# Optimization experiments

Hardware: AMD Instinct MI355X
Metric: run time of the kernel (lower is better)

## Reference

```python
import jax, jax.numpy as jnp
import numpy as np

N, F, H, D = 50000, 128, 8, 16   # nodes, node features, heads, per-head dim (F == H*D -> Identity residual)
E, G = 800000, 512               # edges, graphs
HD = H * D


def _xavier(key, shape):
    fan = sum(shape[-2:]) if len(shape) >= 2 else shape[0] + 1
    lim = (6.0 / (shape[-2] + shape[-1])) ** 0.5 if len(shape) >= 2 else (6.0 / fan) ** 0.5
    return jax.random.uniform(key, shape, jnp.float32, -lim, lim)


def setup_inputs() -> dict:
    key = jax.random.key(0)
    ks = jax.random.split(key, 10)
    x = jax.random.normal(ks[0], (N, F), jnp.float32)
    edge_index = jax.random.randint(ks[1], (2, E), 0, N, dtype=jnp.int64)
    batch = jnp.sort(jax.random.randint(ks[2], (N,), 0, G, dtype=jnp.int64))
    W_src = _xavier(ks[3], (HD, F))
    W_dst = _xavier(ks[4], (HD, F))
    double_attn = _xavier(ks[5], (1, H, D))  # xavier over last two dims
    bias = jnp.zeros((HD,), jnp.float32)
    prelu_alpha = jnp.float32(0.25)          # nn.PReLU() default single weight
    w_weighting = _xavier(ks[6], (1, HD))
    b_weighting = jnp.zeros((1,), jnp.float32)
    w_score = _xavier(ks[7], (HD, HD))
    b_score = jnp.zeros((HD,), jnp.float32)
    return {
        "x": x, "edge_index": edge_index, "batch": batch,
        "W_src": W_src, "W_dst": W_dst, "double_attn": double_attn,
        "bias": bias, "prelu_alpha": prelu_alpha,
        "w_weighting": w_weighting, "b_weighting": b_weighting,
        "w_score": w_score, "b_score": b_score,
    }


def reference(x, edge_index, batch, W_src, W_dst, double_attn, bias, prelu_alpha,
              w_weighting, b_weighting, w_score, b_score):
    src, dst = edge_index[0], edge_index[1]
    # dropout is identity in eval mode
    src_p = (x @ W_src.T).reshape(N, H, D)    # [N,H,D]
    dst_p = (x @ W_dst.T).reshape(N, H, D)
    # edge-wise attention logits: gather + LeakyReLU(0.2) + dot with attention vector
    e = src_p[src] + dst_p[dst]               # [E,H,D]
    e = jnp.where(e > 0, e, 0.2 * e)
    logits = jnp.einsum('ehd,ohd->eh', e, double_attn)  # [E,H] (double_attn has leading 1)
    # segment softmax over destination nodes (global max shift, as in original)
    exp = jnp.exp(logits - logits.max())
    denom = jax.ops.segment_sum(exp, dst, num_segments=N)  # [N,H]
    alpha = exp / (denom[dst] + 1e-16)        # [E,H]
    # weighted aggregation of source projections
    msg = src_p[src] * alpha[:, :, None]      # [E,H,D]
    out = jax.ops.segment_sum(msg, dst, num_segments=N)    # [N,H,D]
    out = out + x.reshape(N, H, D)            # residual (Identity since F == H*D)
    out = out.reshape(N, HD) + bias           # concat heads + bias
    out = jnp.where(out > 0, out, prelu_alpha * out)       # PReLU activation
    # ReadoutPhase: gated sum pooling + max pooling per graph, concatenated
    weighted = jax.nn.sigmoid(out @ w_weighting.T + b_weighting)  # [N,1]
    score = out @ w_score.T + b_score                              # [N,HD]
    g_sum = jax.ops.segment_sum(weighted * score, batch, num_segments=G)  # [G,HD]
    g_max = jax.ops.segment_max(out, batch, num_segments=G)              # [G,HD]
    readout = jnp.concatenate([g_sum, g_max], axis=1)                     # [G,2*HD]
    return out, readout
```

## Files before the change

kernel.cpp:

```cpp
#include <hip/hip_runtime.h>

#define NODES 50000
#define FEAT 128
#define EDGES 800000
#define GRAPHS 512
#define NB 196
#define CHUNK 4096
#define ABLK 196
#define BCAP 8192
#define PROJ_BLOCKS 782

typedef unsigned int u32;
typedef unsigned short u16;
typedef __attribute__((ext_vector_type(8))) short short8;
typedef __attribute__((ext_vector_type(4))) float v4f;
typedef __attribute__((ext_vector_type(4))) u32 u32x4;
typedef __attribute__((ext_vector_type(2))) float f2;

static __device__ __forceinline__ float bflo(u32 u){ return __uint_as_float(u << 16); }
static __device__ __forceinline__ float bfhi(u32 u){ return __uint_as_float(u & 0xffff0000u); }
static __device__ __forceinline__ u16 f2bf(float f){
  u32 u = __float_as_uint(f);
  u32 r = u + 0x7fffu + ((u >> 16) & 1u);
  return (u16)(r >> 16);
}
static __device__ __forceinline__ u32 packbf(float a, float b){
  return (u32)f2bf(a) | ((u32)f2bf(b) << 16);
}
static __device__ __forceinline__ f2 unpk(u32 u){ f2 r; r.x = bflo(u); r.y = bfhi(u); return r; }
static __device__ __forceinline__ f2 vmax2(f2 a, f2 b){ f2 r; r.x = fmaxf(a.x,b.x); r.y = fmaxf(a.y,b.y); return r; }

#define LROW 68
__global__ __launch_bounds__(256) void proj_hist_kernel(
    const float* __restrict__ x, const float* __restrict__ Wsrc,
    const float* __restrict__ Wdst, u16* __restrict__ srcp, u16* __restrict__ dstp,
    const int* __restrict__ ei, int* __restrict__ bcount)
{
  __shared__ u32 x_lds[64 * LROW];
  __shared__ int cnt[NB];
  const int t = threadIdx.x;

  if (blockIdx.x >= PROJ_BLOCKS){
    const int b = blockIdx.x - PROJ_BLOCKS;
    for (int k = t; k < NB; k += 256) cnt[k] = 0;
    __syncthreads();
    const int e0 = b * CHUNK;
    const int e1 = (e0 + CHUNK < EDGES) ? e0 + CHUNK : EDGES;
    for (int e = e0 + t; e < e1; e += 256)
      atomicAdd(&cnt[ei[EDGES + e] >> 8], 1);
    __syncthreads();
    for (int k = t; k < NB; k += 256) bcount[b * NB + k] = cnt[k];
    return;
  }

  const int node0 = blockIdx.x * 64;
  const int rows_valid = NODES - node0 < 64 ? NODES - node0 : 64;
  const float4* xp = (const float4*)(x + (size_t)node0 * 128);
  for (int idx = t; idx < rows_valid * 32; idx += 256){
    const float4 v = xp[idx];
    const int row = idx >> 5, cq = idx & 31;
    x_lds[row * LROW + cq * 2]     = packbf(v.x, v.y);
    x_lds[row * LROW + cq * 2 + 1] = packbf(v.z, v.w);
  }

  const int wave = t >> 6, lane = t & 63;
  const int r16 = lane & 15;
  const int quad = lane >> 4;
  const int ko = quad * 4;
  const int n0 = wave * 32;

  short8 bs[2][4], bd[2][4];
  #pragma unroll
  for (int nt = 0; nt < 2; ++nt){
    const int col = n0 + nt * 16 + r16;
    #pragma unroll
    for (int k = 0; k < 4; ++k){
      const float4* wp = (const float4*)(Wsrc + col * 128 + quad * 8 + k * 32);
      float4 w0 = wp[0], w1 = wp[1];
      u32x4 pk; pk.x = packbf(w0.x,w0.y); pk.y = packbf(w0.z,w0.w);
      pk.z = packbf(w1.x,w1.y); pk.w = packbf(w1.z,w1.w);
      bs[nt][k] = __builtin_bit_cast(short8, pk);
      const float4* vp = (const float4*)(Wdst + col * 128 + quad * 8 + k * 32);
      float4 v0 = vp[0], v1 = vp[1];
      u32x4 qk; qk.x = packbf(v0.x,v0.y); qk.y = packbf(v0.z,v0.w);
      qk.z = packbf(v1.x,v1.y); qk.w = packbf(v1.z,v1.w);
      bd[nt][k] = __builtin_bit_cast(short8, qk);
    }
  }
  __syncthreads();

  #pragma unroll
  for (int mt = 0; mt < 4; ++mt){
    const int node_base = node0 + mt * 16;
    if (node_base >= NODES) break;
    short8 afr[4];
    #pragma unroll
    for (int k = 0; k < 4; ++k)
      afr[k] = *(const short8*)&x_lds[(mt * 16 + r16) * LROW + ko + k * 16];
    v4f s0 = {0.f,0.f,0.f,0.f}, s1 = s0, d0 = s0, d1 = s0;
    #pragma unroll
    for (int k = 0; k < 4; ++k){
      s0 = __builtin_amdgcn_mfma_f32_16x16x32_bf16(afr[k], bs[0][k], s0, 0, 0, 0);
      s1 = __builtin_amdgcn_mfma_f32_16x16x32_bf16(afr[k], bs[1][k], s1, 0, 0, 0);
      d0 = __builtin_amdgcn_mfma_f32_16x16x32_bf16(afr[k], bd[0][k], d0, 0, 0, 0);
      d1 = __builtin_amdgcn_mfma_f32_16x16x32_bf16(afr[k], bd[1][k], d1, 0, 0, 0);
    }
    u16* so = srcp + (size_t)(node_base + quad * 4) * 128 + n0 + r16;
    u16* do_ = dstp + (size_t)(node_base + quad * 4) * 128 + n0 + r16;
    #pragma unroll
    for (int r = 0; r < 4; ++r){
      so[r * 128]      = f2bf(s0[r]);
      so[r * 128 + 16] = f2bf(s1[r]);
      do_[r * 128]      = f2bf(d0[r]);
      do_[r * 128 + 16] = f2bf(d1[r]);
    }
  }
}

__global__ __launch_bounds__(256) void bucket_scatter_kernel(
    const int* __restrict__ ei, const int* __restrict__ bcount,
    int* __restrict__ bstart_g, u32* __restrict__ ebuf)
{
  __shared__ int tot[256];
  __shared__ int bstart_s[NB + 1];
  __shared__ int obase_s[NB];
  __shared__ int cur[NB];
  const int b = blockIdx.x, t = threadIdx.x;
  int total = 0, obase = 0;
  if (t < NB){
    int run = 0;
    for (int q = 0; q < ABLK; ++q){
      if (q == b) obase = run;
      run += bcount[q * NB + t];
    }
    total = run;
  }
  tot[t] = total;
  __syncthreads();
  const int v = total;
  for (int off = 1; off < 256; off <<= 1){
    const int add = (t >= off) ? tot[t - off] : 0;
    __syncthreads();
    tot[t] += add;
    __syncthreads();
  }
  if (t < NB){
    bstart_s[t] = tot[t] - v;
    obase_s[t] = obase;
    cur[t] = 0;
  }
  if (t == NB - 1) bstart_s[NB] = tot[t];
  __syncthreads();
  if (b == 0 && t <= NB) bstart_g[t] = bstart_s[t];

  const int e0 = b * CHUNK;
  const int e1 = (e0 + CHUNK < EDGES) ? e0 + CHUNK : EDGES;
  for (int e = e0 + t; e < e1; e += 256){
    const int d = ei[EDGES + e];
    const int s = ei[e];
    const int k = d >> 8;
    const int r = atomicAdd(&cur[k], 1);
    ebuf[bstart_s[k] + obase_s[k] + r] = (u32)s | ((u32)(d & 255) << 16);
  }
}

__global__ __launch_bounds__(256) void bucket_csr_kernel(
    const u32* __restrict__ ebuf, const int* __restrict__ bstart,
    int* __restrict__ row_start, int* __restrict__ srclist)
{
  __shared__ int cnt[256], excl[256], cur[256];
  __shared__ u32 loc[BCAP];
  const int k = blockIdx.x, t = threadIdx.x;
  const int base = bstart[k];
  int ne = bstart[k + 1] - base;
  if (ne > BCAP) ne = BCAP;
  cnt[t] = 0;
  __syncthreads();
  for (int j = t; j < ne; j += 256)
    atomicAdd(&cnt[(ebuf[base + j] >> 16) & 255], 1);
  __syncthreads();
  const int v = cnt[t];
  for (int off = 1; off < 256; off <<= 1){
    const int add = (t >= off) ? cnt[t - off] : 0;
    __syncthreads();
    cnt[t] += add;
    __syncthreads();
  }
  excl[t] = cnt[t] - v;
  cur[t] = cnt[t] - v;
  __syncthreads();
  const int node = k * 256 + t;
  if (node <= NODES) row_start[node] = base + excl[t];
  for (int j = t; j < ne; j += 256){
    const u32 e = ebuf[base + j];
    const int p = atomicAdd(&cur[(e >> 16) & 255], 1);
    loc[p] = e & 0xFFFFu;
  }
  __syncthreads();
  for (int j = t; j < ne; j += 256)
    srclist[base + j] = (int)loc[j];
}

__global__ __launch_bounds__(256, 4) void aggregate_kernel(
    const u16* __restrict__ srcp, const u16* __restrict__ dstp,
    const int* __restrict__ row_start, const int* __restrict__ srclist,
    const float* __restrict__ x, const float* __restrict__ attn,
    const float* __restrict__ bias, const float* __restrict__ palpha,
    const float* __restrict__ ww, const float* __restrict__ bw,
    float* __restrict__ outp, float* __restrict__ weighted)
{
  const int wv = threadIdx.x >> 6;
  const int lane = threadIdx.x & 63;
  const int half = lane >> 5;
  const int l32 = lane & 31;
  const int h = lane & 7;
  const int es = (lane >> 3) & 3;
  const int i = (blockIdx.x * 4 + wv) * 2 + half;
  const uint4* sp = (const uint4*)srcp;

  f2 d2[8], a2[8];
  {
    const uint4 dA = ((const uint4*)dstp)[(size_t)i * 16 + h * 2];
    const uint4 dB = ((const uint4*)dstp)[(size_t)i * 16 + h * 2 + 1];
    d2[0]=unpk(dA.x); d2[1]=unpk(dA.y); d2[2]=unpk(dA.z); d2[3]=unpk(dA.w);
    d2[4]=unpk(dB.x); d2[5]=unpk(dB.y); d2[6]=unpk(dB.z); d2[7]=unpk(dB.w);
    const float4* ap = (const float4*)attn + h * 4;
    #pragma unroll
    for (int q = 0; q < 4; ++q){
      const float4 vv = ap[q];
      a2[2*q].x = vv.x; a2[2*q].y = vv.y; a2[2*q+1].x = vv.z; a2[2*q+1].y = vv.w;
    }
  }
  const int lo = row_start[i], hi = row_start[i + 1];
  const int deg = hi - lo;
  int myidx = 0;
  if (l32 < deg) myidx = srclist[lo + l32];
  const int nb = (deg + 3) >> 2;
  int nbw = nb;
  { const int ot = __shfl_xor(nb, 32); nbw = nbw > ot ? nbw : ot; }

  f2 acc2[8];
  #pragma unroll
  for (int q = 0; q < 8; ++q){ acc2[q].x = 0.f; acc2[q].y = 0.f; }
  float denom = 0.f;

  auto LOADK = [&](int s, uint4& A, uint4& B){
    const uint4* rp = sp + (size_t)s * 16 + h * 2;
    A = rp[0]; B = rp[1];
  };
  auto COMPV = [&](bool valid, const uint4& A, const uint4& B){
    f2 sv[8];
    sv[0]=unpk(A.x); sv[1]=unpk(A.y); sv[2]=unpk(A.z); sv[3]=unpk(A.w);
    sv[4]=unpk(B.x); sv[5]=unpk(B.y); sv[6]=unpk(B.z); sv[7]=unpk(B.w);
    f2 p; p.x = 0.f; p.y = 0.f;
    #pragma unroll
    for (int q = 0; q < 8; ++q){
      f2 e = sv[q] + d2[q];
      e = vmax2(e, e * 0.2f);
      p += e * a2[q];
    }
    const float w = valid ? __expf(p.x + p.y) : 0.f;
    denom += w;
    f2 w2; w2.x = w; w2.y = w;
    #pragma unroll
    for (int q = 0; q < 8; ++q) acc2[q] += sv[q] * w2;
  };

  int s0,s1,s2,s3,s4,s5,s6,s7;
  {
    int t0;
    t0 = __shfl(myidx, half*32 +  0 + es); s0 = ( 0 + es < deg) ? t0 : 0;
    t0 = __shfl(myidx, half*32 +  4 + es); s1 = ( 4 + es < deg) ? t0 : 0;
    t0 = __shfl(myidx, half*32 +  8 + es); s2 = ( 8 + es < deg) ? t0 : 0;
    t0 = __shfl(myidx, half*32 + 12 + es); s3 = (12 + es < deg) ? t0 : 0;
    t0 = __shfl(myidx, half*32 + 16 + es); s4 = (16 + es < deg) ? t0 : 0;
    t0 = __shfl(myidx, half*32 + 20 + es); s5 = (20 + es < deg) ? t0 : 0;
    t0 = __shfl(myidx, half*32 + 24 + es); s6 = (24 + es < deg) ? t0 : 0;
    t0 = __shfl(myidx, half*32 + 28 + es); s7 = (28 + es < deg) ? t0 : 0;
  }

  uint4 A0,B0,A1,B1,A2,B2,A3,B3;
  if (nbw > 0) LOADK(s0, A0, B0);
  if (nbw > 1) LOADK(s1, A1, B1);
  if (nbw > 2) LOADK(s2, A2, B2);
  if (nbw > 3) LOADK(s3, A3, B3);
  if (nbw > 0){ COMPV( 0 + es < deg, A0, B0); if (nbw > 4) LOADK(s4, A0, B0); }
  if (nbw > 1){ COMPV( 4 + es < deg, A1, B1); if (nbw > 5) LOADK(s5, A1, B1); }
  if (nbw > 2){ COMPV( 8 + es < deg, A2, B2); if (nbw > 6) LOADK(s6, A2, B2); }
  if (nbw > 3){ COMPV(12 + es < deg, A3, B3); if (nbw > 7) LOADK(s7, A3, B3); }
  if (nbw > 4) COMPV(16 + es < deg, A0, B0);
  if (nbw > 5) COMPV(20 + es < deg, A1, B1);
  if (nbw > 6) COMPV(24 + es < deg, A2, B2);
  if (nbw > 7) COMPV(28 + es < deg, A3, B3);
  if (nbw > 8){
    for (int kk = 8; kk < nbw; ++kk){
      const int il = kk * 4 + es;
      const int s = (il < deg) ? srclist[lo + il] : 0;
      uint4 TA, TB;
      LOADK(s, TA, TB);
      COMPV(il < deg, TA, TB);
    }
  }

  #pragma unroll
  for (int m = 8; m <= 16; m <<= 1){
    #pragma unroll
    for (int q = 0; q < 8; ++q){
      acc2[q].x += __shfl_xor(acc2[q].x, m);
      acc2[q].y += __shfl_xor(acc2[q].y, m);
    }
    denom += __shfl_xor(denom, m);
  }
  const float inv = 1.f / (denom + 1e-16f);

  const float al = palpha[0];
  float o[16];
  {
    const float4* xp = (const float4*)x + (size_t)i * 32 + h * 4;
    const float4* bp = (const float4*)bias + h * 4;
    #pragma unroll
    for (int q = 0; q < 4; ++q){
      const float4 xv = xp[q];
      const float4 bv = bp[q];
      float t0 = fmaf(acc2[2*q].x,   inv, xv.x) + bv.x;
      float t1 = fmaf(acc2[2*q].y,   inv, xv.y) + bv.y;
      float t2 = fmaf(acc2[2*q+1].x, inv, xv.z) + bv.z;
      float t3 = fmaf(acc2[2*q+1].y, inv, xv.w) + bv.w;
      o[4*q]   = (t0 > 0.f) ? t0 : al * t0;
      o[4*q+1] = (t1 > 0.f) ? t1 : al * t1;
      o[4*q+2] = (t2 > 0.f) ? t2 : al * t2;
      o[4*q+3] = (t3 > 0.f) ? t3 : al * t3;
    }
  }
  if (es == 0){
    float4* op = (float4*)outp + (size_t)i * 32 + h * 4;
    #pragma unroll
    for (int q = 0; q < 4; ++q){
      float4 vv; vv.x = o[4*q]; vv.y = o[4*q+1]; vv.z = o[4*q+2]; vv.w = o[4*q+3];
      op[q] = vv;
    }
  }
  float z = 0.f;
  {
    const float4* gp = (const float4*)ww + h * 4;
    #pragma unroll
    for (int q = 0; q < 4; ++q){
      const float4 gv = gp[q];
      z = fmaf(o[4*q], gv.x, z); z = fmaf(o[4*q+1], gv.y, z);
      z = fmaf(o[4*q+2], gv.z, z); z = fmaf(o[4*q+3], gv.w, z);
    }
  }
  z += __shfl_xor(z, 1);
  z += __shfl_xor(z, 2);
  z += __shfl_xor(z, 4);
  if (l32 == 0){
    z += bw[0];
    weighted[i] = 1.f / (1.f + __expf(-z));
  }
}

__global__ __launch_bounds__(256) void readout_kernel(
    const float* __restrict__ outp, const float* __restrict__ weighted,
    const int* __restrict__ batchv, const float* __restrict__ wscore,
    const float* __restrict__ bscore, float* __restrict__ ro)
{
  __shared__ int range_s[2];
  __shared__ float wsum_s[128];
  __shared__ float max_s[128];
  __shared__ float wtot_s[2];
  __shared__ float part_s[256];
  const int g = blockIdx.x, t = threadIdx.x;
  const int col = t & 127, grp = t >> 7;
  if (t < 2){
    const int target = g + t;
    int lo = 0, hi = NODES;
    while (lo < hi){ const int m = (lo + hi) >> 1; if (batchv[m] < target) lo = m + 1; else hi = m; }
    range_s[t] = lo;
  }
  __syncthreads();
  const int lo = range_s[0], hi = range_s[1];
  float acc = 0.f, vmax = -INFINITY, wacc = 0.f;
  for (int n = lo + grp; n < hi; n += 2){
    const float w = weighted[n];
    const float v = outp[n * 128 + col];
    acc = fmaf(w, v, acc);
    vmax = fmaxf(vmax, v);
    if (col == 0) wacc += w;
  }
  part_s[t] = acc;
  if (col == 0) wtot_s[grp] = wacc;
  __syncthreads();
  if (grp == 0) wsum_s[col] = acc + part_s[col + 128];
  __syncthreads();
  part_s[t] = vmax;
  __syncthreads();
  if (grp == 0) max_s[col] = fmaxf(vmax, part_s[col + 128]);
  const float wtot = wtot_s[0] + wtot_s[1];
  __syncthreads();
  float dot = 0.f;
  const float* wr = wscore + col * 128 + grp * 64;
  const float* xs = wsum_s + grp * 64;
  #pragma unroll
  for (int k = 0; k < 64; ++k) dot = fmaf(wr[k], xs[k], dot);
  part_s[t] = dot;
  __syncthreads();
  if (grp == 0){
    const float s = dot + part_s[col + 128] + wtot * bscore[col];
    ro[g * 256 + col] = s;
    ro[g * 256 + 128 + col] = max_s[col];
  }
}

extern "C" void kernel_launch(void* const* d_in, const int* in_sizes, int n_in,
                              void* d_out, int out_size, void* d_ws, size_t ws_size,
                              hipStream_t stream)
{
  const float* x      = (const float*)d_in[0];
  const int*   ei     = (const int*)d_in[1];
  const int*   batchv = (const int*)d_in[2];
  const float* Wsrc   = (const float*)d_in[3];
  const float* Wdst   = (const float*)d_in[4];
  const float* attn   = (const float*)d_in[5];
  const float* bias   = (const float*)d_in[6];
  const float* palpha = (const float*)d_in[7];
  const float* ww     = (const float*)d_in[8];
  const float* bw     = (const float*)d_in[9];
  const float* wsc    = (const float*)d_in[10];
  const float* bsc    = (const float*)d_in[11];

  char* ws = (char*)d_ws;
  u16*  srcp      = (u16*) (ws + 0);
  u16*  dstp      = (u16*) (ws + 12800000);
  int*  srclist   = (int*) (ws + 25600000);
  int*  row_start = (int*) (ws + 28800000);
  int*  bcount    = (int*) (ws + 29000192);
  int*  bstart    = (int*) (ws + 29153856);
  float* weighted = (float*)(ws + 29154688);

  float* outp = (float*)d_out;
  float* ro = outp + NODES * FEAT;
  u32* ebuf = (u32*)d_out;

  proj_hist_kernel<<<PROJ_BLOCKS + ABLK, 256, 0, stream>>>(
      x, Wsrc, Wdst, srcp, dstp, ei, bcount);
  bucket_scatter_kernel<<<ABLK, 256, 0, stream>>>(ei, bcount, bstart, ebuf);
  bucket_csr_kernel<<<NB, 256, 0, stream>>>(ebuf, bstart, row_start, srclist);
  aggregate_kernel<<<6250, 256, 0, stream>>>(srcp, dstp, row_start, srclist,
                                             x, attn, bias, palpha, ww, bw,
                                             outp, weighted);
  readout_kernel<<<GRAPHS, 256, 0, stream>>>(outp, weighted, batchv, wsc, bsc, ro);
}
```

Before: 214.2 us.

## Sort nodes by degree within buckets and store source list as u16

```diff
diff --git a/kernel.cpp b/kernel.cpp
--- a/kernel.cpp
+++ b/kernel.cpp
@@ -166,15 +166,18 @@
 
 __global__ __launch_bounds__(256) void bucket_csr_kernel(
     const u32* __restrict__ ebuf, const int* __restrict__ bstart,
-    int* __restrict__ row_start, int* __restrict__ srclist)
+    int* __restrict__ row_start, u16* __restrict__ srclist,
+    int* __restrict__ perm)
 {
   __shared__ int cnt[256], excl[256], cur[256];
   __shared__ u32 loc[BCAP];
+  __shared__ int bins[64], boff[64];
   const int k = blockIdx.x, t = threadIdx.x;
   const int base = bstart[k];
   int ne = bstart[k + 1] - base;
   if (ne > BCAP) ne = BCAP;
   cnt[t] = 0;
+  if (t < 64) bins[t] = 0;
   __syncthreads();
   for (int j = t; j < ne; j += 256)
     atomicAdd(&cnt[(ebuf[base + j] >> 16) & 255], 1);
@@ -198,12 +201,28 @@
   }
   __syncthreads();
   for (int j = t; j < ne; j += 256)
-    srclist[base + j] = (int)loc[j];
+    srclist[base + j] = (u16)loc[j];
+
+  const bool realn = node < NODES;
+  const int degc = v < 63 ? v : 63;
+  if (realn) atomicAdd(&bins[degc], 1);
+  __syncthreads();
+  if (t == 0){
+    int run = 0;
+    #pragma unroll
+    for (int q = 0; q < 64; ++q){ boff[q] = run; run += bins[q]; }
+  }
+  __syncthreads();
+  if (realn){
+    const int r = atomicAdd(&boff[degc], 1);
+    perm[k * 256 + r] = node;
+  }
 }
 
 __global__ __launch_bounds__(256, 4) void aggregate_kernel(
     const u16* __restrict__ srcp, const u16* __restrict__ dstp,
-    const int* __restrict__ row_start, const int* __restrict__ srclist,
+    const int* __restrict__ row_start, const u16* __restrict__ srclist,
+    const int* __restrict__ perm,
     const float* __restrict__ x, const float* __restrict__ attn,
     const float* __restrict__ bias, const float* __restrict__ palpha,
     const float* __restrict__ ww, const float* __restrict__ bw,
@@ -215,7 +234,7 @@
   const int l32 = lane & 31;
   const int h = lane & 7;
   const int es = (lane >> 3) & 3;
-  const int i = (blockIdx.x * 4 + wv) * 2 + half;
+  const int i = perm[(blockIdx.x * 4 + wv) * 2 + half];
   const uint4* sp = (const uint4*)srcp;
 
   f2 d2[8], a2[8];
@@ -234,7 +253,7 @@
   const int lo = row_start[i], hi = row_start[i + 1];
   const int deg = hi - lo;
   int myidx = 0;
-  if (l32 < deg) myidx = srclist[lo + l32];
+  if (l32 < deg) myidx = (int)srclist[lo + l32];
   const int nb = (deg + 3) >> 2;
   int nbw = nb;
   { const int ot = __shfl_xor(nb, 32); nbw = nbw > ot ? nbw : ot; }
@@ -295,7 +314,7 @@
   if (nbw > 8){
     for (int kk = 8; kk < nbw; ++kk){
       const int il = kk * 4 + es;
-      const int s = (il < deg) ? srclist[lo + il] : 0;
+      const int s = (il < deg) ? (int)srclist[lo + il] : 0;
       uint4 TA, TB;
       LOADK(s, TA, TB);
       COMPV(il < deg, TA, TB);
@@ -431,7 +450,8 @@
   char* ws = (char*)d_ws;
   u16*  srcp      = (u16*) (ws + 0);
   u16*  dstp      = (u16*) (ws + 12800000);
-  int*  srclist   = (int*) (ws + 25600000);
+  u16*  srclist   = (u16*) (ws + 25600000);
+  int*  perm      = (int*) (ws + 27200000);
   int*  row_start = (int*) (ws + 28800000);
   int*  bcount    = (int*) (ws + 29000192);
   int*  bstart    = (int*) (ws + 29153856);
@@ -444,8 +464,8 @@
   proj_hist_kernel<<<PROJ_BLOCKS + ABLK, 256, 0, stream>>>(
       x, Wsrc, Wdst, srcp, dstp, ei, bcount);
   bucket_scatter_kernel<<<ABLK, 256, 0, stream>>>(ei, bcount, bstart, ebuf);
-  bucket_csr_kernel<<<NB, 256, 0, stream>>>(ebuf, bstart, row_start, srclist);
-  aggregate_kernel<<<6250, 256, 0, stream>>>(srcp, dstp, row_start, srclist,
+  bucket_csr_kernel<<<NB, 256, 0, stream>>>(ebuf, bstart, row_start, srclist, perm);
+  aggregate_kernel<<<6250, 256, 0, stream>>>(srcp, dstp, row_start, srclist, perm,
                                              x, attn, bias, palpha, ww, bw,
                                              outp, weighted);
   readout_kernel<<<GRAPHS, 256, 0, stream>>>(outp, weighted, batchv, wsc, bsc, ro);
```

New measurement: 223.0 us. +4.1%, slower.
